# Kernel optimization log

Hardware: AMD Instinct MI355X
Metric: run time of the kernel (lower is better)

## Reference

```python
import jax, jax.numpy as jnp
import numpy as np

D = 768
H = 8
HD = D // H
MLP = 3072
EPS = 1e-5


def _ln(x, g, b):
    mu = jnp.mean(x, axis=-1, keepdims=True)
    var = jnp.var(x, axis=-1, keepdims=True)
    return (x - mu) * jax.lax.rsqrt(var + EPS) * g + b


def setup_inputs() -> dict:
    key = jax.random.key(0)
    ks = jax.random.split(key, 20)
    B, N = 4, 2048
    s = 0.02
    inp = {
        "x": jax.random.normal(ks[0], (B, N, D), jnp.float32),
        "position_bias": jax.random.normal(ks[1], (N, N), jnp.float32),
        "wq": jax.random.normal(ks[2], (D, D), jnp.float32) * s,
        "bq": jnp.zeros((D,), jnp.float32),
        "wk": jax.random.normal(ks[3], (D, D), jnp.float32) * s,
        "bk": jnp.zeros((D,), jnp.float32),
        "wv": jax.random.normal(ks[4], (D, D), jnp.float32) * s,
        "bv": jnp.zeros((D,), jnp.float32),
        "wo": jax.random.normal(ks[5], (D, D), jnp.float32) * s,
        "bo": jnp.zeros((D,), jnp.float32),
        "g1": jnp.ones((D,), jnp.float32),
        "b1": jnp.zeros((D,), jnp.float32),
        "g2": jnp.ones((D,), jnp.float32),
        "b2": jnp.zeros((D,), jnp.float32),
        "w_ff1": jax.random.normal(ks[6], (D, MLP), jnp.float32) * s,
        "b_ff1": jnp.zeros((MLP,), jnp.float32),
        "w_ff2": jax.random.normal(ks[7], (MLP, D), jnp.float32) * s,
        "b_ff2": jnp.zeros((D,), jnp.float32),
    }
    return inp


def reference(x, position_bias, wq, bq, wk, bk, wv, bv, wo, bo, g1, b1, g2, b2, w_ff1, b_ff1, w_ff2, b_ff2):
    B, N, _ = x.shape
    scale = HD ** -0.5
    # pre-norm attention
    n1 = _ln(x, g1, b1)
    q = (n1 @ wq + bq).reshape(B, N, H, HD).transpose(0, 2, 1, 3)
    k = (n1 @ wk + bk).reshape(B, N, H, HD).transpose(0, 2, 1, 3)
    v = (n1 @ wv + bv).reshape(B, N, H, HD).transpose(0, 2, 1, 3)
    attn = jnp.einsum('bhqd,bhkd->bhqk', q, k) * scale  # [B,H,N,N]
    attn = attn + position_bias[None, None, :, :]
    attn = jax.nn.softmax(attn, axis=-1)
    out = jnp.einsum('bhqk,bhkd->bhqd', attn, v)
    out = out.transpose(0, 2, 1, 3).reshape(B, N, D)
    out = out @ wo + bo
    x = x + out
    # pre-norm GELU MLP (exact erf gelu, torch default)
    n2 = _ln(x, g2, b2)
    h = jax.nn.gelu(n2 @ w_ff1 + b_ff1, approximate=False)
    x = x + (h @ w_ff2 + b_ff2)
    return x
```

## Files before the change

### kernel.cpp

```cpp
#include <hip/hip_runtime.h>
#include <hip/hip_bf16.h>

#define D 768
#define H 8
#define HD 96
#define MLP 3072
#define NB 2048
#define BATCH 4

typedef __attribute__((ext_vector_type(8))) short short8;
typedef __attribute__((ext_vector_type(4))) short short4v;
typedef __attribute__((ext_vector_type(4))) float f32x4;
typedef __attribute__((ext_vector_type(16))) float f32x16;
typedef __attribute__((ext_vector_type(4))) int int4v;

typedef const __attribute__((address_space(1))) unsigned int gu32;
typedef __attribute__((address_space(3))) unsigned int lu32;

__device__ inline void gload16(const void* g, void* l){
  __builtin_amdgcn_global_load_lds((gu32*)g, (lu32*)l, 16, 0, 0);
}

__device__ inline short f2b(float f){
  __hip_bfloat16 h = __float2bfloat16(f);
  return *reinterpret_cast<short*>(&h);
}
__device__ inline float b2f(short s){
  return __uint_as_float(((unsigned)(unsigned short)s) << 16);
}
__device__ inline float fexp2(float x){ return __builtin_amdgcn_exp2f(x); }

__device__ inline unsigned cvtpk(float lo, float hi){
  unsigned r;
  asm volatile("v_cvt_pk_bf16_f32 %0, %1, %2" : "=v"(r) : "v"(lo), "v"(hi));
  return r;
}

__global__ __launch_bounds__(256) void wtrans(const float* __restrict__ in, short* __restrict__ out, int K, int Nc){
  __shared__ float tile[32][33];
  int bk = blockIdx.x, bn = blockIdx.y;
  int tx = threadIdx.x & 31, ty = threadIdx.x >> 5;
  #pragma unroll
  for (int i=0;i<4;++i)
    tile[ty + i*8][tx] = in[(size_t)(bk*32 + ty + i*8)*Nc + bn*32 + tx];
  __syncthreads();
  #pragma unroll
  for (int i=0;i<4;++i)
    out[(size_t)(bn*32 + ty + i*8)*K + bk*32 + tx] = f2b(tile[tx][ty + i*8]);
}

__global__ __launch_bounds__(256) void bias_cat(const float* __restrict__ bq, const float* __restrict__ bk,
                                                const float* __restrict__ bv, float* __restrict__ o){
  int i = blockIdx.x*256 + threadIdx.x;
  if (i < 768){ o[i]=bq[i]; o[768+i]=bk[i]; o[1536+i]=bv[i]; }
}

__global__ __launch_bounds__(256) void pb_reorg(const float* __restrict__ pb, short* __restrict__ pbT){
  int qt = blockIdx.x, kb = blockIdx.y;
  int t = threadIdx.x;
  int l = t >> 2;
  int vbase = (t & 3) * 8;
  int q = qt*32 + (l & 31);
  int hi = l >> 5;
  const float L2E = 1.4426950408889634f;
  short8 o;
  #pragma unroll
  for (int j=0;j<8;++j){
    int v = vbase + j;
    int r = v & 15, tile = v >> 4;
    int k = kb*64 + tile*32 + 8*(r>>2) + (r&3) + 4*hi;
    o[j] = f2b(pb[(size_t)q*NB + k] * L2E);
  }
  *(short8*)&pbT[(((size_t)(qt*32 + kb))*64 + l)*32 + vbase] = o;
}

__global__ __launch_bounds__(256) void ln_k(const float* __restrict__ X, const float* __restrict__ gg,
                                            const float* __restrict__ bb, short* __restrict__ out){
  int row = blockIdx.x, t = threadIdx.x;
  const float* x = X + (size_t)row*D;
  float v0=x[t], v1=x[t+256], v2=x[t+512];
  float s=v0+v1+v2, ss=v0*v0+v1*v1+v2*v2;
  #pragma unroll
  for (int m=1;m<64;m<<=1){ s += __shfl_xor(s,m); ss += __shfl_xor(ss,m); }
  __shared__ float red[8];
  int w=t>>6, lane=t&63;
  if (!lane){ red[w]=s; red[4+w]=ss; }
  __syncthreads();
  s = red[0]+red[1]+red[2]+red[3];
  ss = red[4]+red[5]+red[6]+red[7];
  float mu = s*(1.f/768.f);
  float inv = rsqrtf(ss*(1.f/768.f) - mu*mu + 1e-5f);
  short* o = out + (size_t)row*D;
  o[t]     = f2b((v0-mu)*inv*gg[t]     + bb[t]);
  o[t+256] = f2b((v1-mu)*inv*gg[t+256] + bb[t+256]);
  o[t+512] = f2b((v2-mu)*inv*gg[t+512] + bb[t+512]);
}

template<int MODE>
__global__ __launch_bounds__(256) void gemm_bt(
    const short* __restrict__ A, const short* __restrict__ Bt,
    const float* __restrict__ bias, const float* __restrict__ resid,
    void* __restrict__ Cout, int Nc, int K)
{
  __shared__ __align__(16) short As[128][32];
  __shared__ __align__(16) short Bs[128][32];
  int m0 = blockIdx.x*128, n0 = blockIdx.y*128;
  int t = threadIdx.x;
  int lane = t & 63, w = t >> 6;
  int wm = w >> 1, wn = w & 1;
  int r = lane & 15, g = lane >> 4;
  const short* aSrc = A  + (size_t)(m0 + (t>>2))*K + (t&3)*8;
  const short* bSrc = Bt + (size_t)(n0 + (t>>2))*K + (t&3)*8;
  char* aDst0 = (char*)As + w*1024;
  char* aDst1 = (char*)As + 4096 + w*1024;
  char* bDst0 = (char*)Bs + w*1024;
  char* bDst1 = (char*)Bs + 4096 + w*1024;
  size_t rowK64 = (size_t)64*K;
  f32x4 acc[4][4] = {};
  for (int kt=0; kt<K; kt+=32){
    gload16(aSrc + kt,          aDst0);
    gload16(aSrc + kt + rowK64, aDst1);
    gload16(bSrc + kt,          bDst0);
    gload16(bSrc + kt + rowK64, bDst1);
    __syncthreads();
    short8 af[4], bfr[4];
    #pragma unroll
    for (int i=0;i<4;++i){
      af[i]  = *(const short8*)&As[wm*64 + i*16 + r][g*8];
      bfr[i] = *(const short8*)&Bs[wn*64 + i*16 + r][g*8];
    }
    #pragma unroll
    for (int i=0;i<4;++i)
      #pragma unroll
      for (int j=0;j<4;++j)
        acc[i][j] = __builtin_amdgcn_mfma_f32_16x16x32_bf16(af[i], bfr[j], acc[i][j], 0,0,0);
    __syncthreads();
  }
  #pragma unroll
  for (int i=0;i<4;++i){
    #pragma unroll
    for (int j=0;j<4;++j){
      int col = n0 + wn*64 + j*16 + r;
      float bv = bias[col];
      #pragma unroll
      for (int q=0;q<4;++q){
        int row = m0 + wm*64 + i*16 + g*4 + q;
        size_t idx = (size_t)row*Nc + col;
        float val = acc[i][j][q] + bv;
        if constexpr (MODE==0){
          ((short*)Cout)[idx] = f2b(val);
        } else if constexpr (MODE==2){
          float ge = 0.5f*val*(1.f + erff(val*0.70710678118654752f));
          ((short*)Cout)[idx] = f2b(ge);
        }
      }
    }
  }
}

template<int MODE>
__global__ __launch_bounds__(256) void gemm64(
    const short* __restrict__ A, const short* __restrict__ Bt,
    const float* __restrict__ bias, const float* __restrict__ resid,
    void* __restrict__ Cout, int Nc, int K)
{
  __shared__ __align__(16) short As[64][32];
  __shared__ __align__(16) short Bs[128][32];
  int m0 = blockIdx.x*64, n0 = blockIdx.y*128;
  int t = threadIdx.x;
  int lane = t & 63, w = t >> 6;
  int r = lane & 15, g = lane >> 4;
  const short* aSrc = A  + (size_t)(m0 + (t>>2))*K + (t&3)*8;
  const short* bSrc = Bt + (size_t)(n0 + (t>>2))*K + (t&3)*8;
  char* aDst  = (char*)As + w*1024;
  char* bDst0 = (char*)Bs + w*1024;
  char* bDst1 = (char*)Bs + 4096 + w*1024;
  size_t rowK64 = (size_t)64*K;
  f32x4 acc[4][2] = {};
  for (int kt=0; kt<K; kt+=32){
    gload16(aSrc + kt,          aDst);
    gload16(bSrc + kt,          bDst0);
    gload16(bSrc + kt + rowK64, bDst1);
    __syncthreads();
    short8 af[4], bfr[2];
    #pragma unroll
    for (int i=0;i<4;++i) af[i] = *(const short8*)&As[i*16 + r][g*8];
    #pragma unroll
    for (int j=0;j<2;++j) bfr[j] = *(const short8*)&Bs[w*32 + j*16 + r][g*8];
    #pragma unroll
    for (int i=0;i<4;++i)
      #pragma unroll
      for (int j=0;j<2;++j)
        acc[i][j] = __builtin_amdgcn_mfma_f32_16x16x32_bf16(af[i], bfr[j], acc[i][j], 0,0,0);
    __syncthreads();
  }
  #pragma unroll
  for (int i=0;i<4;++i){
    #pragma unroll
    for (int j=0;j<2;++j){
      int col = n0 + w*32 + j*16 + r;
      #pragma unroll
      for (int q=0;q<4;++q){
        int row = m0 + i*16 + g*4 + q;
        if constexpr (MODE==1){
          size_t idx = (size_t)row*Nc + col;
          ((float*)Cout)[idx] = acc[i][j][q] + bias[col] + resid[idx];
        } else {
          int hh = row / 96, hd = row - hh*96;
          int bb = col >> 11, nn = col & 2047;
          size_t idx = ((size_t)((bb*8 + hh)*96 + hd))*2048 + nn;
          ((short*)Cout)[idx] = f2b(acc[i][j][q] + bias[row]);
        }
      }
    }
  }
}

__global__ __launch_bounds__(512, 1) void attn_k(const short* __restrict__ qkv, const short* __restrict__ v_t,
                                                 const short* __restrict__ pbT, short* __restrict__ aout){
  int bx = blockIdx.x;
  int h = bx & 7, b = (bx>>3)&3, qb = bx>>5;
  int t = threadIdx.x, l = t & 63, w = t >> 6;
  int l31 = l & 31, hi = l >> 5, l7 = l & 7;
  __shared__ __align__(16) short Ks[2][64][128];
  __shared__ __align__(16) short Vs[96][64];
  const float SCALE2 = 0.10206207261596575f * 1.4426950408889634f;

  int qRow = qb*256 + w*32 + l31;
  const short* qg = qkv + (size_t)(b*NB + qRow)*1536 + h*HD;
  short8 qa[6];
  #pragma unroll
  for (int ds=0; ds<6; ++ds)
    qa[ds] = *(const short8*)&qg[ds*16 + hi*8];

  f32x16 oacc[3] = {};
  float m_run = -3.0e38f, l_run = 0.f;

  int r0 = t/12,        c0 = t%12;
  int s1 = 512 + t;
  int r1 = s1/12,       c1 = s1%12;
  int ldsK0 = r0*128 + (c0 ^ (r0&7))*8;
  int ldsK1 = r1*128 + (c1 ^ (r1&7))*8;
  const short* kgB = qkv + (size_t)(b*NB)*1536 + 768 + h*HD;
  bool wlow = (t < 256);
  int vr0 = t>>3,  vc0 = t&7;
  int vr1 = (512+t)>>3, vc1 = (512+t)&7;
  const short* vgB = v_t + (size_t)((b*H+h)*HD)*NB;
  const short* vsrc0 = vgB + (size_t)vr0*NB + (vc0 ^ (vr0&7))*8;
  const short* vsrc1 = vgB + (size_t)vr1*NB + (vc1 ^ (vr1&7))*8;
  char* vdst0 = (char*)Vs + w*1024;
  char* vdst1 = (char*)Vs + 8192 + w*1024;
  const short* pbB = pbT + (((size_t)((qb*8 + w)*32))*64 + l)*32;

  {
    short8 ka = *(const short8*)&kgB[(size_t)r0*1536 + c0*8];
    short* ks0 = &Ks[0][0][0];
    *(short8*)(ks0 + ldsK0) = ka;
    if (wlow){
      short8 kb = *(const short8*)&kgB[(size_t)r1*1536 + c1*8];
      *(short8*)(ks0 + ldsK1) = kb;
    }
  }
  __syncthreads();

  for (int kt=0; kt<32; ++kt){
    int cur = kt & 1;
    int kbase = kt*64;
    const short* pbk = pbB + kt*2048;
    short8 pbr0 = *(const short8*)&pbk[0];
    short8 pbr1 = *(const short8*)&pbk[8];
    short8 pbr2 = *(const short8*)&pbk[16];
    short8 pbr3 = *(const short8*)&pbk[24];
    gload16(vsrc0 + kbase, vdst0);
    if (wlow) gload16(vsrc1 + kbase, vdst1);
    int kb2 = (kt < 31) ? (kbase + 64) : kbase;
    short8 kra = *(const short8*)&kgB[(size_t)(kb2 + r0)*1536 + c0*8];
    short8 krb = {};
    if (wlow) krb = *(const short8*)&kgB[(size_t)(kb2 + r1)*1536 + c1*8];

    f32x16 sacc[2] = {};
    __builtin_amdgcn_s_setprio(1);
    #pragma unroll
    for (int tt=0; tt<2; ++tt){
      #pragma unroll
      for (int ds=0; ds<6; ++ds){
        short8 kf = *(const short8*)&Ks[cur][tt*32 + l31][((ds*2 + hi) ^ l7)*8];
        sacc[tt] = __builtin_amdgcn_mfma_f32_32x32x16_bf16(kf, qa[ds], sacc[tt], 0,0,0);
      }
    }
    __builtin_amdgcn_s_setprio(0);

    float vals[2][16];
    #pragma unroll
    for (int tt=0; tt<2; ++tt)
      #pragma unroll
      for (int r=0; r<16; ++r){
        int v = tt*16 + r;
        short pv = (v<8)?pbr0[v]:(v<16)?pbr1[v-8]:(v<24)?pbr2[v-16]:pbr3[v-24];
        vals[tt][r] = fmaf(sacc[tt][r], SCALE2, b2f(pv));
      }
    float pm = vals[0][0];
    #pragma unroll
    for (int tt=0; tt<2; ++tt)
      #pragma unroll
      for (int r=0; r<16; ++r) pm = fmaxf(pm, vals[tt][r]);
    pm = fmaxf(pm, __shfl_xor(pm, 32));
    if (__any(pm - m_run > 8.f)){
      float mn = fmaxf(m_run, pm);
      float f = fexp2(m_run - mn);
      l_run *= f; m_run = mn;
      int fi = __float_as_int(f);
      #pragma unroll
      for (int reg=0; reg<16; ++reg){
        int q = (reg&3) + 8*(reg>>2) + 4*hi;
        float fr = __int_as_float(__builtin_amdgcn_ds_bpermute(q<<2, fi));
        oacc[0][reg] *= fr; oacc[1][reg] *= fr; oacc[2][reg] *= fr;
      }
    }
    float p[2][16];
    float rs = 0.f;
    #pragma unroll
    for (int tt=0; tt<2; ++tt)
      #pragma unroll
      for (int r=0; r<16; ++r){
        p[tt][r] = fexp2(vals[tt][r] - m_run);
        rs += p[tt][r];
      }
    rs += __shfl_xor(rs, 32);
    l_run += rs;

    short8 pa[4];
    #pragma unroll
    for (int ks=0; ks<4; ++ks){
      int tt = ks>>1;
      int rb = (ks&1)*8;
      unsigned G0a = cvtpk(p[tt][rb+0], p[tt][rb+1]);
      unsigned G0b = cvtpk(p[tt][rb+2], p[tt][rb+3]);
      unsigned G1a = cvtpk(p[tt][rb+4], p[tt][rb+5]);
      unsigned G1b = cvtpk(p[tt][rb+6], p[tt][rb+7]);
      unsigned sG0a = (unsigned)__shfl_xor((int)G0a, 32);
      unsigned sG0b = (unsigned)__shfl_xor((int)G0b, 32);
      unsigned sG1a = (unsigned)__shfl_xor((int)G1a, 32);
      unsigned sG1b = (unsigned)__shfl_xor((int)G1b, 32);
      int4v wv;
      wv[0] = hi ? (int)sG1a : (int)G0a;
      wv[1] = hi ? (int)sG1b : (int)G0b;
      wv[2] = hi ? (int)G1a  : (int)sG0a;
      wv[3] = hi ? (int)G1b  : (int)sG0b;
      pa[ks] = __builtin_bit_cast(short8, wv);
    }

    __syncthreads();

    __builtin_amdgcn_s_setprio(1);
    #pragma unroll
    for (int dt=0; dt<3; ++dt){
      #pragma unroll
      for (int ks=0; ks<4; ++ks){
        short8 vb = *(const short8*)&Vs[dt*32 + l31][((ks*2 + hi) ^ l7)*8];
        oacc[dt] = __builtin_amdgcn_mfma_f32_32x32x16_bf16(pa[ks], vb, oacc[dt], 0,0,0);
      }
    }
    __builtin_amdgcn_s_setprio(0);

    if (kt < 31){
      short* ksn = &Ks[cur^1][0][0];
      *(short8*)(ksn + ldsK0) = kra;
      if (wlow) *(short8*)(ksn + ldsK1) = krb;
      __syncthreads();
    }
  }

  float inv_self = 1.f / l_run;
  int ii = __float_as_int(inv_self);
  #pragma unroll
  for (int reg=0; reg<16; ++reg){
    int q = (reg&3) + 8*(reg>>2) + 4*hi;
    float invq = __int_as_float(__builtin_amdgcn_ds_bpermute(q<<2, ii));
    int rowg = b*NB + qb*256 + w*32 + q;
    #pragma unroll
    for (int dt=0; dt<3; ++dt){
      int col = h*HD + dt*32 + l31;
      aout[(size_t)rowg*D + col] = f2b(oacc[dt][reg] * invq);
    }
  }
}

extern "C" void kernel_launch(void* const* d_in, const int* in_sizes, int n_in,
                              void* d_out, int out_size, void* d_ws, size_t ws_size,
                              hipStream_t stream){
  const float* x   = (const float*)d_in[0];
  const float* pb  = (const float*)d_in[1];
  const float* wq  = (const float*)d_in[2];
  const float* bq  = (const float*)d_in[3];
  const float* wk  = (const float*)d_in[4];
  const float* bk  = (const float*)d_in[5];
  const float* wv  = (const float*)d_in[6];
  const float* bv  = (const float*)d_in[7];
  const float* wo  = (const float*)d_in[8];
  const float* bo  = (const float*)d_in[9];
  const float* g1  = (const float*)d_in[10];
  const float* b1  = (const float*)d_in[11];
  const float* g2  = (const float*)d_in[12];
  const float* b2  = (const float*)d_in[13];
  const float* wf1 = (const float*)d_in[14];
  const float* bf1 = (const float*)d_in[15];
  const float* wf2 = (const float*)d_in[16];
  const float* bf2 = (const float*)d_in[17];
  float* out = (float*)d_out;

  char* p = (char*)d_ws;
  auto alloc = [&](size_t bytes){ char* q = p; p += (bytes + 255) & ~(size_t)255; return q; };
  short* wqkv_t = (short*)alloc((size_t)2304*768*2);
  short* wo_t   = (short*)alloc((size_t)768*768*2);
  short* w1_t   = (short*)alloc((size_t)3072*768*2);
  short* w2_t   = (short*)alloc((size_t)768*3072*2);
  float* bqkv   = (float*)alloc(2304*4);
  short* pbT    = (short*)alloc((size_t)2048*2048*2);
  float* x1     = (float*)alloc((size_t)8192*768*4);
  short* n2     = (short*)alloc((size_t)8192*768*2);
  short* n1     = (short*)alloc((size_t)8192*768*2);
  short* qkv    = (short*)alloc((size_t)8192*1536*2);
  short* v_t    = (short*)alloc((size_t)32*96*2048*2);
  short* hbuf   = n1;
  short* attn_o = n1;
  short* wv_t   = wqkv_t + (size_t)2*768*768;

  wtrans<<<dim3(24,24),256,0,stream>>>(wq, wqkv_t,           768, 768);
  wtrans<<<dim3(24,24),256,0,stream>>>(wk, wqkv_t + 768*768, 768, 768);
  wtrans<<<dim3(24,24),256,0,stream>>>(wv, wv_t,             768, 768);
  wtrans<<<dim3(24,24),256,0,stream>>>(wo, wo_t, 768, 768);
  wtrans<<<dim3(24,96),256,0,stream>>>(wf1, w1_t, 768, 3072);
  wtrans<<<dim3(96,24),256,0,stream>>>(wf2, w2_t, 3072, 768);
  bias_cat<<<3,256,0,stream>>>(bq,bk,bv,bqkv);
  pb_reorg<<<dim3(64,32),256,0,stream>>>(pb, pbT);
  ln_k<<<8192,256,0,stream>>>(x, g1, b1, n1);
  gemm_bt<0><<<dim3(64,12),256,0,stream>>>(n1, wqkv_t, bqkv, nullptr, qkv, 1536, 768);
  gemm64<5><<<dim3(12,64),256,0,stream>>>(wv_t, n1, bv, nullptr, v_t, 0, 768);
  attn_k<<<256,512,0,stream>>>(qkv, v_t, pbT, attn_o);
  gemm64<1><<<dim3(128,6),256,0,stream>>>(attn_o, wo_t, bo, x, x1, 768, 768);
  ln_k<<<8192,256,0,stream>>>(x1, g2, b2, n2);
  gemm_bt<2><<<dim3(64,24),256,0,stream>>>(n2, w1_t, bf1, nullptr, hbuf, 3072, 768);
  gemm64<1><<<dim3(128,6),256,0,stream>>>(hbuf, w2_t, bf2, x1, out, 768, 3072);
}
```

Baseline: 338.4 us.

## Split attention blocks to 128 query rows with 256 threads, three blocks per CU

The attention kernel now launches 512 blocks of 256 threads, each covering 128 query rows, where it previously launched 256 blocks of 512 threads covering 256 rows. K and V tile staging is redistributed so each thread loads three chunks, and the launch bounds allow three resident blocks per CU. The aim is to fill the 256 CUs better than one block per CU and to overlap blocks with each other. In exchange, every K/V tile is loaded twice as often across the grid, which adds global traffic and per-thread register pressure.

```diff
diff --git a/kernel.cpp b/kernel.cpp
--- a/kernel.cpp
+++ b/kernel.cpp
@@ -216,7 +216,7 @@
   }
 }
 
-__global__ __launch_bounds__(512, 1) void attn_k(const short* __restrict__ qkv, const short* __restrict__ v_t,
+__global__ __launch_bounds__(256, 3) void attn_k(const short* __restrict__ qkv, const short* __restrict__ v_t,
                                                  const short* __restrict__ pbT, short* __restrict__ aout){
   int bx = blockIdx.x;
   int h = bx & 7, b = (bx>>3)&3, qb = bx>>5;
@@ -226,7 +226,7 @@
   __shared__ __align__(16) short Vs[96][64];
   const float SCALE2 = 0.10206207261596575f * 1.4426950408889634f;
 
-  int qRow = qb*256 + w*32 + l31;
+  int qRow = qb*128 + w*32 + l31;
   const short* qg = qkv + (size_t)(b*NB + qRow)*1536 + h*HD;
   short8 qa[6];
   #pragma unroll
@@ -236,29 +236,32 @@
   f32x16 oacc[3] = {};
   float m_run = -3.0e38f, l_run = 0.f;
 
-  int r0 = t/12,        c0 = t%12;
-  int s1 = 512 + t;
-  int r1 = s1/12,       c1 = s1%12;
-  int ldsK0 = r0*128 + (c0 ^ (r0&7))*8;
-  int ldsK1 = r1*128 + (c1 ^ (r1&7))*8;
+  int kr[3], kc[3], ldsK[3];
+  #pragma unroll
+  for (int i=0;i<3;++i){
+    int s = i*256 + t;
+    kr[i] = s/12; kc[i] = s%12;
+    ldsK[i] = kr[i]*128 + (kc[i] ^ (kr[i]&7))*8;
+  }
   const short* kgB = qkv + (size_t)(b*NB)*1536 + 768 + h*HD;
-  bool wlow = (t < 256);
-  int vr0 = t>>3,  vc0 = t&7;
-  int vr1 = (512+t)>>3, vc1 = (512+t)&7;
   const short* vgB = v_t + (size_t)((b*H+h)*HD)*NB;
-  const short* vsrc0 = vgB + (size_t)vr0*NB + (vc0 ^ (vr0&7))*8;
-  const short* vsrc1 = vgB + (size_t)vr1*NB + (vc1 ^ (vr1&7))*8;
-  char* vdst0 = (char*)Vs + w*1024;
-  char* vdst1 = (char*)Vs + 8192 + w*1024;
-  const short* pbB = pbT + (((size_t)((qb*8 + w)*32))*64 + l)*32;
+  const short* vsrc[3];
+  char* vdst[3];
+  #pragma unroll
+  for (int i=0;i<3;++i){
+    int s = i*256 + t;
+    int vr = s>>3, vc = s&7;
+    vsrc[i] = vgB + (size_t)vr*NB + (vc ^ (vr&7))*8;
+    vdst[i] = (char*)Vs + (i*256 + w*64)*16;
+  }
+  const short* pbB = pbT + (((size_t)((qb*4 + w)*32))*64 + l)*32;
 
   {
-    short8 ka = *(const short8*)&kgB[(size_t)r0*1536 + c0*8];
     short* ks0 = &Ks[0][0][0];
-    *(short8*)(ks0 + ldsK0) = ka;
-    if (wlow){
-      short8 kb = *(const short8*)&kgB[(size_t)r1*1536 + c1*8];
-      *(short8*)(ks0 + ldsK1) = kb;
+    #pragma unroll
+    for (int i=0;i<3;++i){
+      short8 ka = *(const short8*)&kgB[(size_t)kr[i]*1536 + kc[i]*8];
+      *(short8*)(ks0 + ldsK[i]) = ka;
     }
   }
   __syncthreads();
@@ -271,12 +274,14 @@
     short8 pbr1 = *(const short8*)&pbk[8];
     short8 pbr2 = *(const short8*)&pbk[16];
     short8 pbr3 = *(const short8*)&pbk[24];
-    gload16(vsrc0 + kbase, vdst0);
-    if (wlow) gload16(vsrc1 + kbase, vdst1);
+    #pragma unroll
+    for (int i=0;i<3;++i)
+      gload16(vsrc[i] + kbase, vdst[i]);
     int kb2 = (kt < 31) ? (kbase + 64) : kbase;
-    short8 kra = *(const short8*)&kgB[(size_t)(kb2 + r0)*1536 + c0*8];
-    short8 krb = {};
-    if (wlow) krb = *(const short8*)&kgB[(size_t)(kb2 + r1)*1536 + c1*8];
+    short8 kra[3];
+    #pragma unroll
+    for (int i=0;i<3;++i)
+      kra[i] = *(const short8*)&kgB[(size_t)(kb2 + kr[i])*1536 + kc[i]*8];
 
     f32x16 sacc[2] = {};
     __builtin_amdgcn_s_setprio(1);
@@ -365,8 +370,9 @@
 
     if (kt < 31){
       short* ksn = &Ks[cur^1][0][0];
-      *(short8*)(ksn + ldsK0) = kra;
-      if (wlow) *(short8*)(ksn + ldsK1) = krb;
+      #pragma unroll
+      for (int i=0;i<3;++i)
+        *(short8*)(ksn + ldsK[i]) = kra[i];
       __syncthreads();
     }
   }
@@ -377,7 +383,7 @@
   for (int reg=0; reg<16; ++reg){
     int q = (reg&3) + 8*(reg>>2) + 4*hi;
     float invq = __int_as_float(__builtin_amdgcn_ds_bpermute(q<<2, ii));
-    int rowg = b*NB + qb*256 + w*32 + q;
+    int rowg = b*NB + qb*128 + w*32 + q;
     #pragma unroll
     for (int dt=0; dt<3; ++dt){
       int col = h*HD + dt*32 + l31;
@@ -437,7 +443,7 @@
   ln_k<<<8192,256,0,stream>>>(x, g1, b1, n1);
   gemm_bt<0><<<dim3(64,12),256,0,stream>>>(n1, wqkv_t, bqkv, nullptr, qkv, 1536, 768);
   gemm64<5><<<dim3(12,64),256,0,stream>>>(wv_t, n1, bv, nullptr, v_t, 0, 768);
-  attn_k<<<256,512,0,stream>>>(qkv, v_t, pbT, attn_o);
+  attn_k<<<512,256,0,stream>>>(qkv, v_t, pbT, attn_o);
   gemm64<1><<<dim3(128,6),256,0,stream>>>(attn_o, wo_t, bo, x, x1, 768, 768);
   ln_k<<<8192,256,0,stream>>>(x1, g2, b2, n2);
   gemm_bt<2><<<dim3(64,24),256,0,stream>>>(n2, w1_t, bf1, nullptr, hbuf, 3072, 768);
```

Result: no change. 339.8 us (+0.4%).

## Double-buffer LDS tiles in GEMM kernels to overlap global loads with MFMA

Applied to the files above, without the earlier changes.

Both GEMM kernels (gemm_bt and gemm64) now keep two LDS stages. The next K-tile is prefetched via global_load_lds while the current tile is consumed, and partial vmcnt waits replace the full syncthreads. The goal is to hide global memory latency behind the MFMA work in the K loop. The cost is twice the LDS per block, which may lower occupancy, plus hand-written waitcnt and barrier logic that depends on the compiler's instruction ordering.

```diff
diff --git a/kernel.cpp b/kernel.cpp
--- a/kernel.cpp
+++ b/kernel.cpp
@@ -102,8 +102,8 @@
     const float* __restrict__ bias, const float* __restrict__ resid,
     void* __restrict__ Cout, int Nc, int K)
 {
-  __shared__ __align__(16) short As[128][32];
-  __shared__ __align__(16) short Bs[128][32];
+  __shared__ __align__(16) short As[2][128][32];
+  __shared__ __align__(16) short Bs[2][128][32];
   int m0 = blockIdx.x*128, n0 = blockIdx.y*128;
   int t = threadIdx.x;
   int lane = t & 63, w = t >> 6;
@@ -111,30 +111,43 @@
   int r = lane & 15, g = lane >> 4;
   const short* aSrc = A  + (size_t)(m0 + (t>>2))*K + (t&3)*8;
   const short* bSrc = Bt + (size_t)(n0 + (t>>2))*K + (t&3)*8;
-  char* aDst0 = (char*)As + w*1024;
-  char* aDst1 = (char*)As + 4096 + w*1024;
-  char* bDst0 = (char*)Bs + w*1024;
-  char* bDst1 = (char*)Bs + 4096 + w*1024;
   size_t rowK64 = (size_t)64*K;
+  int dstOff = w*1024;
   f32x4 acc[4][4] = {};
-  for (int kt=0; kt<K; kt+=32){
-    gload16(aSrc + kt,          aDst0);
-    gload16(aSrc + kt + rowK64, aDst1);
-    gload16(bSrc + kt,          bDst0);
-    gload16(bSrc + kt + rowK64, bDst1);
-    __syncthreads();
+  int nst = K >> 5;
+  gload16(aSrc,          (char*)As + dstOff);
+  gload16(aSrc + rowK64, (char*)As + 4096 + dstOff);
+  gload16(bSrc,          (char*)Bs + dstOff);
+  gload16(bSrc + rowK64, (char*)Bs + 4096 + dstOff);
+  for (int it=0; it<nst; ++it){
+    int cur = it & 1;
+    if (it+1 < nst){
+      int kt = (it+1)*32;
+      char* ab = (char*)As + (cur^1)*8192;
+      char* bb = (char*)Bs + (cur^1)*8192;
+      gload16(aSrc + kt,          ab + dstOff);
+      gload16(aSrc + kt + rowK64, ab + 4096 + dstOff);
+      gload16(bSrc + kt,          bb + dstOff);
+      gload16(bSrc + kt + rowK64, bb + 4096 + dstOff);
+      asm volatile("s_waitcnt vmcnt(4)" ::: "memory");
+    } else {
+      asm volatile("s_waitcnt vmcnt(0)" ::: "memory");
+    }
+    __builtin_amdgcn_s_barrier();
+    __builtin_amdgcn_sched_barrier(0);
     short8 af[4], bfr[4];
     #pragma unroll
     for (int i=0;i<4;++i){
-      af[i]  = *(const short8*)&As[wm*64 + i*16 + r][g*8];
-      bfr[i] = *(const short8*)&Bs[wn*64 + i*16 + r][g*8];
+      af[i]  = *(const short8*)&As[cur][wm*64 + i*16 + r][g*8];
+      bfr[i] = *(const short8*)&Bs[cur][wn*64 + i*16 + r][g*8];
     }
     #pragma unroll
     for (int i=0;i<4;++i)
       #pragma unroll
       for (int j=0;j<4;++j)
         acc[i][j] = __builtin_amdgcn_mfma_f32_16x16x32_bf16(af[i], bfr[j], acc[i][j], 0,0,0);
-    __syncthreads();
+    __builtin_amdgcn_sched_barrier(0);
+    __builtin_amdgcn_s_barrier();
   }
   #pragma unroll
   for (int i=0;i<4;++i){
@@ -164,35 +177,48 @@
     const float* __restrict__ bias, const float* __restrict__ resid,
     void* __restrict__ Cout, int Nc, int K)
 {
-  __shared__ __align__(16) short As[64][32];
-  __shared__ __align__(16) short Bs[128][32];
+  __shared__ __align__(16) short As[2][64][32];
+  __shared__ __align__(16) short Bs[2][128][32];
   int m0 = blockIdx.x*64, n0 = blockIdx.y*128;
   int t = threadIdx.x;
   int lane = t & 63, w = t >> 6;
   int r = lane & 15, g = lane >> 4;
   const short* aSrc = A  + (size_t)(m0 + (t>>2))*K + (t&3)*8;
   const short* bSrc = Bt + (size_t)(n0 + (t>>2))*K + (t&3)*8;
-  char* aDst  = (char*)As + w*1024;
-  char* bDst0 = (char*)Bs + w*1024;
-  char* bDst1 = (char*)Bs + 4096 + w*1024;
   size_t rowK64 = (size_t)64*K;
+  int dstOff = w*1024;
   f32x4 acc[4][2] = {};
-  for (int kt=0; kt<K; kt+=32){
-    gload16(aSrc + kt,          aDst);
-    gload16(bSrc + kt,          bDst0);
-    gload16(bSrc + kt + rowK64, bDst1);
-    __syncthreads();
+  int nst = K >> 5;
+  gload16(aSrc,          (char*)As + dstOff);
+  gload16(bSrc,          (char*)Bs + dstOff);
+  gload16(bSrc + rowK64, (char*)Bs + 4096 + dstOff);
+  for (int it=0; it<nst; ++it){
+    int cur = it & 1;
+    if (it+1 < nst){
+      int kt = (it+1)*32;
+      char* ab = (char*)As + (cur^1)*4096;
+      char* bb = (char*)Bs + (cur^1)*8192;
+      gload16(aSrc + kt,          ab + dstOff);
+      gload16(bSrc + kt,          bb + dstOff);
+      gload16(bSrc + kt + rowK64, bb + 4096 + dstOff);
+      asm volatile("s_waitcnt vmcnt(3)" ::: "memory");
+    } else {
+      asm volatile("s_waitcnt vmcnt(0)" ::: "memory");
+    }
+    __builtin_amdgcn_s_barrier();
+    __builtin_amdgcn_sched_barrier(0);
     short8 af[4], bfr[2];
     #pragma unroll
-    for (int i=0;i<4;++i) af[i] = *(const short8*)&As[i*16 + r][g*8];
-    #pragma unroll
-    for (int j=0;j<2;++j) bfr[j] = *(const short8*)&Bs[w*32 + j*16 + r][g*8];
+    for (int i=0;i<4;++i) af[i] = *(const short8*)&As[cur][i*16 + r][g*8];
+    #pragma unroll
+    for (int j=0;j<2;++j) bfr[j] = *(const short8*)&Bs[cur][w*32 + j*16 + r][g*8];
     #pragma unroll
     for (int i=0;i<4;++i)
       #pragma unroll
       for (int j=0;j<2;++j)
         acc[i][j] = __builtin_amdgcn_mfma_f32_16x16x32_bf16(af[i], bfr[j], acc[i][j], 0,0,0);
-    __syncthreads();
+    __builtin_amdgcn_sched_barrier(0);
+    __builtin_amdgcn_s_barrier();
   }
   #pragma unroll
   for (int i=0;i<4;++i){
```

Measured after the change: 324.9 us. 1.04x faster.
